# Kernel optimization log

Hardware: AMD Instinct MI355X
Metric: run time of the kernel (lower is better)

The kernel has to match this reference:

```python
import jax, jax.numpy as jnp
import numpy as np

LAMBDA_1 = 1.0
LAMBDA_2 = 0.5


def setup_inputs() -> dict:
    key = jax.random.key(0)
    k1, k2, k3, k4, k5 = jax.random.split(key, 5)
    N_TRAIN, N_UNL, C = 4096, 32768, 1000
    G, K = 512, 64
    return {
        "train_logits": jax.random.normal(k1, (N_TRAIN, C), dtype=jnp.float32),
        "train_targets": jax.random.randint(k2, (N_TRAIN,), 0, C, dtype=jnp.int64),
        "unlabeled_logits": jax.random.normal(k3, (N_UNL, C), dtype=jnp.float32),
        "centroid_ids": jax.random.randint(k4, (G,), 0, N_TRAIN, dtype=jnp.int64),
        "member_ids": jax.random.randint(k5, (G, K), 0, N_UNL, dtype=jnp.int64),
    }


def reference(train_logits, train_targets, unlabeled_logits, centroid_ids, member_ids):
    N_unl = unlabeled_logits.shape[0]
    G, K = member_ids.shape

    # --- cross-entropy (mean) ---
    logp = jax.nn.log_softmax(train_logits, axis=-1)
    ce = -jnp.mean(jnp.take_along_axis(logp, train_targets[:, None], axis=1))

    # --- gather group tensors ---
    centroids = train_logits[centroid_ids]          # [G, C]
    members = unlabeled_logits[member_ids]          # [G, K, C]

    # --- alignment: sum_g sum_k ||centroid_g - member_gk||_2 / N_unl ---
    align = jnp.sum(jnp.linalg.norm(centroids[:, None, :] - members, axis=-1)) / N_unl

    # --- robustness: per-group upper-triangle pairwise L2 sums / (K * N_unl) ---
    sq = jnp.sum(members * members, axis=-1)                       # [G, K]
    gram = jnp.einsum("gkc,glc->gkl", members, members)            # [G, K, K]
    d2 = jnp.maximum(sq[:, :, None] + sq[:, None, :] - 2.0 * gram, 0.0)
    dist = jnp.sqrt(jnp.where(d2 > 0, d2, 1.0)) * (d2 > 0)         # safe sqrt
    iu = jnp.triu(jnp.ones((K, K), dtype=dist.dtype), k=1)         # i < j pairs
    robust = jnp.sum(dist * iu) / (K * N_unl)

    return ce + LAMBDA_1 * align + LAMBDA_2 * robust
```

## Files before the change

### kernel.cpp

```cpp
#include <hip/hip_runtime.h>

#define N_TRAIN 4096
#define N_UNL   32768
#define C_DIM   1000
#define G_GRP   512
#define K_MEM   64

#define CE_BLOCKS (N_TRAIN / 16)
#define NPART     (G_GRP + CE_BLOCKS)

#define PITCH_B 528
#define ROWS    80

typedef short        short8 __attribute__((ext_vector_type(8)));
typedef float        f32x4  __attribute__((ext_vector_type(4)));
typedef unsigned int u32x4  __attribute__((ext_vector_type(4)));

__device__ __forceinline__ unsigned int pack_bf(float a, float b) {
    unsigned int ua = __float_as_uint(a) + 0x8000u;
    unsigned int ub = __float_as_uint(b) + 0x8000u;
    return (ua >> 16) | (ub & 0xffff0000u);
}

__global__ __launch_bounds__(256) void fused_kernel(const float* __restrict__ train,
                                                    const int*   __restrict__ targets,
                                                    const float* __restrict__ unl,
                                                    const int*   __restrict__ cids,
                                                    const int*   __restrict__ mids,
                                                    float* __restrict__ part) {
    __shared__ __align__(16) unsigned short bf[ROWS * (PITCH_B / 2)];
    __shared__ int   ids_sh[K_MEM];
    __shared__ float sq_sh[K_MEM];
    __shared__ float red_sh[256];
    __shared__ float sqc_sh;

    const int tid  = threadIdx.x;
    const int w    = tid >> 6;
    const int lane = tid & 63;

    if (blockIdx.x >= G_GRP) {
        const int blk = (int)blockIdx.x - G_GRP;
        float ce = 0.f;
        for (int r4 = 0; r4 < 4; ++r4) {
            const int row = blk * 16 + w * 4 + r4;
            const float* rp = train + (long)row * C_DIM;
            float x[16];
#pragma unroll
            for (int i = 0; i < 16; ++i) {
                int c = lane + i * 64;
                x[i] = (c < C_DIM) ? rp[c] : -1e30f;
            }
            float m = x[0];
#pragma unroll
            for (int i = 1; i < 16; ++i) m = fmaxf(m, x[i]);
#pragma unroll
            for (int off = 32; off > 0; off >>= 1) m = fmaxf(m, __shfl_xor(m, off, 64));
            float s = 0.f;
#pragma unroll
            for (int i = 0; i < 16; ++i) s += __expf(x[i] - m);
#pragma unroll
            for (int off = 32; off > 0; off >>= 1) s += __shfl_xor(s, off, 64);
            if (lane == 0) {
                int t = targets[row];
                ce += -(rp[t] - m - __logf(s));
            }
        }
        if (lane == 0) red_sh[w] = ce;
        __syncthreads();
        if (tid == 0)
            part[G_GRP + blk] = (red_sh[0] + red_sh[1] + red_sh[2] + red_sh[3]) *
                                (1.0f / (float)N_TRAIN);
        return;
    }

    const int g    = blockIdx.x;
    const int quad = lane >> 4;
    const int c16  = lane & 15;

    for (int idx = tid; idx < 495; idx += 256)
        *(u32x4*)((char*)bf + 65 * PITCH_B + idx * 16) = (u32x4){0, 0, 0, 0};
    if (tid < K_MEM) ids_sh[tid] = mids[g * K_MEM + tid];
    __syncthreads();

    const int rgrp = tid >> 5;
    const int l32  = tid & 31;
    const int colf = l32 * 8;
    const int cid  = cids[g];

    const float* srcb[8];
#pragma unroll
    for (int i = 0; i < 8; ++i)
        srcb[i] = unl + (long)ids_sh[rgrp + 8 * i] * C_DIM + colf;
    const float* csrc = train + (long)cid * C_DIM + colf;

    f32x4 acc[4], accC, accD;
#pragma unroll
    for (int t = 0; t < 4; ++t) acc[t] = (f32x4){0.f, 0.f, 0.f, 0.f};
    accC = (f32x4){0.f, 0.f, 0.f, 0.f};
    accD = (f32x4){0.f, 0.f, 0.f, 0.f};

    const float4 z4 = make_float4(0.f, 0.f, 0.f, 0.f);

    for (int ch = 0; ch < 4; ++ch) {
        const int col = ch * 256 + colf;
        const bool v0 = (col < C_DIM);
        const bool v1 = (col + 4 < C_DIM);
#pragma unroll
        for (int i = 0; i < 8; ++i) {
            float4 a = v0 ? *(const float4*)(srcb[i] + ch * 256) : z4;
            float4 b = v1 ? *(const float4*)(srcb[i] + ch * 256 + 4) : z4;
            u32x4 h = {pack_bf(a.x, a.y), pack_bf(a.z, a.w),
                       pack_bf(b.x, b.y), pack_bf(b.z, b.w)};
            *(u32x4*)((char*)bf + (rgrp + 8 * i) * PITCH_B + colf * 2) = h;
        }
        if (tid < 32) {
            float4 a = v0 ? *(const float4*)(csrc + ch * 256) : z4;
            float4 b = v1 ? *(const float4*)(csrc + ch * 256 + 4) : z4;
            u32x4 h = {pack_bf(a.x, a.y), pack_bf(a.z, a.w),
                       pack_bf(b.x, b.y), pack_bf(b.z, b.w)};
            *(u32x4*)((char*)bf + 64 * PITCH_B + colf * 2) = h;
        }
        __syncthreads();

#pragma unroll
        for (int s = 0; s < 8; ++s) {
            const int kbb = s * 64 + quad * 16;
            const char* base = (const char*)bf;
            short8 b0 = *(const short8*)(base + (0 * 16 + c16) * PITCH_B + kbb);
            short8 b1 = *(const short8*)(base + (1 * 16 + c16) * PITCH_B + kbb);
            short8 b2 = *(const short8*)(base + (2 * 16 + c16) * PITCH_B + kbb);
            short8 b3 = *(const short8*)(base + (3 * 16 + c16) * PITCH_B + kbb);
            short8 aM = *(const short8*)(base + (w * 16 + c16) * PITCH_B + kbb);
            short8 aC = *(const short8*)(base + (64 + c16) * PITCH_B + kbb);
            acc[0] = __builtin_amdgcn_mfma_f32_16x16x32_bf16(aM, b0, acc[0], 0, 0, 0);
            acc[1] = __builtin_amdgcn_mfma_f32_16x16x32_bf16(aM, b1, acc[1], 0, 0, 0);
            acc[2] = __builtin_amdgcn_mfma_f32_16x16x32_bf16(aM, b2, acc[2], 0, 0, 0);
            acc[3] = __builtin_amdgcn_mfma_f32_16x16x32_bf16(aM, b3, acc[3], 0, 0, 0);
            accC   = __builtin_amdgcn_mfma_f32_16x16x32_bf16(aC, aM, accC, 0, 0, 0);
            if (w == 0)
                accD = __builtin_amdgcn_mfma_f32_16x16x32_bf16(aC, aC, accD, 0, 0, 0);
        }
        __syncthreads();
    }

#pragma unroll
    for (int t = 0; t < 4; ++t) {
        if (t == w) {
#pragma unroll
            for (int r = 0; r < 4; ++r)
                if (c16 == quad * 4 + r) sq_sh[w * 16 + c16] = acc[t][r];
        }
    }
    if (tid == 0) sqc_sh = accD[0];
    __syncthreads();

    float local = 0.f;
    if (quad == 0) {
        const int j = w * 16 + c16;
        const float d2 = sqc_sh + sq_sh[j] - 2.f * accC[0];
        if (d2 > 0.f) local += sqrtf(d2) * (1.0f / (float)N_UNL);
    }
#pragma unroll
    for (int t = 0; t < 4; ++t) {
#pragma unroll
        for (int r = 0; r < 4; ++r) {
            const int i = w * 16 + quad * 4 + r;
            const int j = t * 16 + c16;
            if (j > i) {
                const float d2 = sq_sh[i] + sq_sh[j] - 2.f * acc[t][r];
                if (d2 > 0.f)
                    local += sqrtf(d2) * (0.5f / ((float)K_MEM * (float)N_UNL));
            }
        }
    }

    red_sh[tid] = local;
    __syncthreads();
#pragma unroll
    for (int s = 128; s > 0; s >>= 1) {
        if (tid < s) red_sh[tid] += red_sh[tid + s];
        __syncthreads();
    }
    if (tid == 0) part[g] = red_sh[0];
}

__global__ __launch_bounds__(256) void final_kernel(const float* __restrict__ part,
                                                    float* __restrict__ out, int out_size) {
    __shared__ float red[256];
    float s = 0.f;
    for (int i = threadIdx.x; i < NPART; i += 256) s += part[i];
    red[threadIdx.x] = s;
    __syncthreads();
#pragma unroll
    for (int st = 128; st > 0; st >>= 1) {
        if (threadIdx.x < st) red[threadIdx.x] += red[threadIdx.x + st];
        __syncthreads();
    }
    if (threadIdx.x == 0) out[0] = red[0];
    for (int i = 1 + threadIdx.x; i < out_size; i += 256) out[i] = 0.f;
}

extern "C" void kernel_launch(void* const* d_in, const int* in_sizes, int n_in,
                              void* d_out, int out_size, void* d_ws, size_t ws_size,
                              hipStream_t stream) {
    (void)in_sizes; (void)n_in; (void)ws_size;
    const float* train_logits  = (const float*)d_in[0];
    const int*   train_targets = (const int*)d_in[1];
    const float* unl           = (const float*)d_in[2];
    const int*   centroid_ids  = (const int*)d_in[3];
    const int*   member_ids    = (const int*)d_in[4];
    float* out  = (float*)d_out;
    float* part = (float*)d_ws;

    fused_kernel<<<NPART, 256, 0, stream>>>(train_logits, train_targets, unl,
                                            centroid_ids, member_ids, part);
    final_kernel<<<1, 256, 0, stream>>>(part, out, out_size);
}
```

Baseline: 217.1 us.

## Prefetch next chunk into registers, halve LDS tile, replace final reduction with atomics

After: 210.4 us. 3.1% less time.

```diff
diff --git a/kernel.cpp b/kernel.cpp
--- a/kernel.cpp
+++ b/kernel.cpp
@@ -7,13 +7,16 @@
 #define K_MEM   64
 
 #define CE_BLOCKS (N_TRAIN / 16)
-#define NPART     (G_GRP + CE_BLOCKS)
-
-#define PITCH_B 528
+#define NBLK      (G_GRP + CE_BLOCKS)
+
+#define CHUNKS  8
+#define CCOLS   128
+#define PITCH_B 272
 #define ROWS    80
 
 typedef short        short8 __attribute__((ext_vector_type(8)));
 typedef float        f32x4  __attribute__((ext_vector_type(4)));
+typedef unsigned int u32x2  __attribute__((ext_vector_type(2)));
 typedef unsigned int u32x4  __attribute__((ext_vector_type(4)));
 
 __device__ __forceinline__ unsigned int pack_bf(float a, float b) {
@@ -27,7 +30,7 @@
                                                     const float* __restrict__ unl,
                                                     const int*   __restrict__ cids,
                                                     const int*   __restrict__ mids,
-                                                    float* __restrict__ part) {
+                                                    float* __restrict__ out) {
     __shared__ __align__(16) unsigned short bf[ROWS * (PITCH_B / 2)];
     __shared__ int   ids_sh[K_MEM];
     __shared__ float sq_sh[K_MEM];
@@ -68,8 +71,8 @@
         if (lane == 0) red_sh[w] = ce;
         __syncthreads();
         if (tid == 0)
-            part[G_GRP + blk] = (red_sh[0] + red_sh[1] + red_sh[2] + red_sh[3]) *
-                                (1.0f / (float)N_TRAIN);
+            atomicAdd(out, (red_sh[0] + red_sh[1] + red_sh[2] + red_sh[3]) *
+                           (1.0f / (float)N_TRAIN));
         return;
     }
 
@@ -77,21 +80,20 @@
     const int quad = lane >> 4;
     const int c16  = lane & 15;
 
-    for (int idx = tid; idx < 495; idx += 256)
-        *(u32x4*)((char*)bf + 65 * PITCH_B + idx * 16) = (u32x4){0, 0, 0, 0};
+    if (tid < 255)
+        *(u32x4*)((char*)bf + 65 * PITCH_B + tid * 16) = (u32x4){0, 0, 0, 0};
     if (tid < K_MEM) ids_sh[tid] = mids[g * K_MEM + tid];
     __syncthreads();
 
     const int rgrp = tid >> 5;
     const int l32  = tid & 31;
-    const int colf = l32 * 8;
     const int cid  = cids[g];
 
     const float* srcb[8];
 #pragma unroll
     for (int i = 0; i < 8; ++i)
-        srcb[i] = unl + (long)ids_sh[rgrp + 8 * i] * C_DIM + colf;
-    const float* csrc = train + (long)cid * C_DIM + colf;
+        srcb[i] = unl + (long)ids_sh[rgrp + 8 * i] * C_DIM + l32 * 4;
+    const float* csrc = train + (long)cid * C_DIM + l32 * 4;
 
     f32x4 acc[4], accC, accD;
 #pragma unroll
@@ -101,29 +103,41 @@
 
     const float4 z4 = make_float4(0.f, 0.f, 0.f, 0.f);
 
-    for (int ch = 0; ch < 4; ++ch) {
-        const int col = ch * 256 + colf;
-        const bool v0 = (col < C_DIM);
-        const bool v1 = (col + 4 < C_DIM);
+    float4 mreg[8];
+    float4 creg;
+
+    {
+        const bool v = (l32 * 4 < C_DIM);
+#pragma unroll
+        for (int i = 0; i < 8; ++i) mreg[i] = v ? *(const float4*)(srcb[i]) : z4;
+        if (tid < 32) creg = *(const float4*)(csrc);
+    }
+
+    for (int ch = 0; ch < CHUNKS; ++ch) {
+        __syncthreads();
+
 #pragma unroll
         for (int i = 0; i < 8; ++i) {
-            float4 a = v0 ? *(const float4*)(srcb[i] + ch * 256) : z4;
-            float4 b = v1 ? *(const float4*)(srcb[i] + ch * 256 + 4) : z4;
-            u32x4 h = {pack_bf(a.x, a.y), pack_bf(a.z, a.w),
-                       pack_bf(b.x, b.y), pack_bf(b.z, b.w)};
-            *(u32x4*)((char*)bf + (rgrp + 8 * i) * PITCH_B + colf * 2) = h;
+            u32x2 h = {pack_bf(mreg[i].x, mreg[i].y), pack_bf(mreg[i].z, mreg[i].w)};
+            *(u32x2*)((char*)bf + (rgrp + 8 * i) * PITCH_B + l32 * 8) = h;
         }
         if (tid < 32) {
-            float4 a = v0 ? *(const float4*)(csrc + ch * 256) : z4;
-            float4 b = v1 ? *(const float4*)(csrc + ch * 256 + 4) : z4;
-            u32x4 h = {pack_bf(a.x, a.y), pack_bf(a.z, a.w),
-                       pack_bf(b.x, b.y), pack_bf(b.z, b.w)};
-            *(u32x4*)((char*)bf + 64 * PITCH_B + colf * 2) = h;
-        }
-        __syncthreads();
-
-#pragma unroll
-        for (int s = 0; s < 8; ++s) {
+            u32x2 h = {pack_bf(creg.x, creg.y), pack_bf(creg.z, creg.w)};
+            *(u32x2*)((char*)bf + 64 * PITCH_B + tid * 8) = h;
+        }
+        __syncthreads();
+
+        if (ch + 1 < CHUNKS) {
+            const int col = (ch + 1) * CCOLS + l32 * 4;
+            const bool v = (col < C_DIM);
+            const long off = (long)(ch + 1) * CCOLS;
+#pragma unroll
+            for (int i = 0; i < 8; ++i) mreg[i] = v ? *(const float4*)(srcb[i] + off) : z4;
+            if (tid < 32) creg = v ? *(const float4*)(csrc + off) : z4;
+        }
+
+#pragma unroll
+        for (int s = 0; s < 4; ++s) {
             const int kbb = s * 64 + quad * 16;
             const char* base = (const char*)bf;
             short8 b0 = *(const short8*)(base + (0 * 16 + c16) * PITCH_B + kbb);
@@ -140,7 +154,6 @@
             if (w == 0)
                 accD = __builtin_amdgcn_mfma_f32_16x16x32_bf16(aC, aC, accD, 0, 0, 0);
         }
-        __syncthreads();
     }
 
 #pragma unroll
@@ -181,38 +194,21 @@
         if (tid < s) red_sh[tid] += red_sh[tid + s];
         __syncthreads();
     }
-    if (tid == 0) part[g] = red_sh[0];
-}
-
-__global__ __launch_bounds__(256) void final_kernel(const float* __restrict__ part,
-                                                    float* __restrict__ out, int out_size) {
-    __shared__ float red[256];
-    float s = 0.f;
-    for (int i = threadIdx.x; i < NPART; i += 256) s += part[i];
-    red[threadIdx.x] = s;
-    __syncthreads();
-#pragma unroll
-    for (int st = 128; st > 0; st >>= 1) {
-        if (threadIdx.x < st) red[threadIdx.x] += red[threadIdx.x + st];
-        __syncthreads();
-    }
-    if (threadIdx.x == 0) out[0] = red[0];
-    for (int i = 1 + threadIdx.x; i < out_size; i += 256) out[i] = 0.f;
+    if (tid == 0) atomicAdd(out, red_sh[0]);
 }
 
 extern "C" void kernel_launch(void* const* d_in, const int* in_sizes, int n_in,
                               void* d_out, int out_size, void* d_ws, size_t ws_size,
                               hipStream_t stream) {
-    (void)in_sizes; (void)n_in; (void)ws_size;
+    (void)in_sizes; (void)n_in; (void)d_ws; (void)ws_size;
     const float* train_logits  = (const float*)d_in[0];
     const int*   train_targets = (const int*)d_in[1];
     const float* unl           = (const float*)d_in[2];
     const int*   centroid_ids  = (const int*)d_in[3];
     const int*   member_ids    = (const int*)d_in[4];
-    float* out  = (float*)d_out;
-    float* part = (float*)d_ws;
-
-    fused_kernel<<<NPART, 256, 0, stream>>>(train_logits, train_targets, unl,
-                                            centroid_ids, member_ids, part);
-    final_kernel<<<1, 256, 0, stream>>>(part, out, out_size);
+    float* out = (float*)d_out;
+
+    hipMemsetAsync(out, 0, (size_t)out_size * sizeof(float), stream);
+    fused_kernel<<<NBLK, 256, 0, stream>>>(train_logits, train_targets, unl,
+                                           centroid_ids, member_ids, out);
 }
```
